# Kernel optimization log

Measured on AMD Instinct MI355X. Metric: run time of the kernel, lower is better.

Reference implementation:

```python
import jax, jax.numpy as jnp
import numpy as np

S = 95      # spatial cube size
B = 2       # batch (events)
C0 = 8      # init_conv_nplanes
C1 = 16     # planes after one downsample (inplanes*2)
K = 3       # kernel size (init conv, basic blocks, downsample)
STR = 2     # downsample stride
EPS = 1e-4  # scn BatchNorm eps
N = 40000   # total active voxels


def conv3d(x, w, stride, padding):
    # x: [B,D,H,W,Cin], w: [k,k,k,Cin,Cout]
    return jax.lax.conv_general_dilated(x, w, (stride,) * 3, padding,
                                        dimension_numbers=('NDHWC', 'DHWIO', 'NDHWC'))


def masked_bn(x, mask, gamma, beta, relu):
    # scn.BatchNorm(ReLU): per-channel stats over ACTIVE sites only
    n = jnp.maximum(mask.sum(), 1.0)
    mean = (x * mask).sum(axis=(0, 1, 2, 3)) / n
    var = (((x - mean) ** 2) * mask).sum(axis=(0, 1, 2, 3)) / n
    y = (x - mean) * jax.lax.rsqrt(var + EPS) * gamma + beta
    if relu:
        y = jnp.maximum(y, 0.0)
    return y * mask


def basic(x, mask, g1, b1, w1, g2, b2, w2):
    # pre-activation ResidualBlock_basic; submanifold convs keep the active-site mask
    y = masked_bn(x, mask, g1, b1, True)
    y = conv3d(y, w1, 1, 'SAME') * mask
    y = masked_bn(y, mask, g2, b2, True)
    y = conv3d(y, w2, 1, 'SAME') * mask
    return x + y


def downsample(x, mask, g1, b1, w1, g2, b2, w2, w3):
    # ResidualBlock_downsample: BNReLU -> {strided conv -> BNReLU -> submanifold conv} + {strided conv}
    y = masked_bn(x, mask, g1, b1, True)
    new_mask = jax.lax.reduce_window(mask, 0.0, jax.lax.max,
                                     (1, K, K, K, 1), (1, STR, STR, STR, 1), 'VALID')
    y1 = conv3d(y, w1, STR, 'VALID') * new_mask
    y1 = masked_bn(y1, new_mask, g2, b2, True)
    y1 = conv3d(y1, w2, 1, 'SAME') * new_mask
    y2 = conv3d(y, w3, STR, 'VALID') * new_mask
    return y1 + y2, new_mask


def _forward(coords, feats, w0, g0, b0,
             ba0_g1, ba0_b1, ba0_w1, ba0_g2, ba0_b2, ba0_w2,
             ba1_g1, ba1_b1, ba1_w1, ba1_g2, ba1_b2, ba1_w2,
             bo0_g1, bo0_b1, bo0_w1, bo0_g2, bo0_b2, bo0_w2,
             bo1_g1, bo1_b1, bo1_w1, bo1_g2, bo1_b2, bo1_w2,
             dn_g1, dn_b1, dn_w1, dn_g2, dn_b2, dn_w2, dn_w3,
             l1_w, l1_b, l2_w, l2_b):
    bi, xi, yi, zi = coords[:, 3], coords[:, 0], coords[:, 1], coords[:, 2]
    # scn.InputLayer: scatter (summing duplicates) into dense grid; inactive sites are exactly 0
    grid = jnp.zeros((B, S, S, S, 1), jnp.float32).at[bi, xi, yi, zi].add(feats)
    mask = jnp.zeros((B, S, S, S, 1), jnp.float32).at[bi, xi, yi, zi, 0].set(1.0)
    # ConvBNBlock: submanifold conv + BN + ReLU
    x = conv3d(grid, w0, 1, 'SAME') * mask
    x = masked_bn(x, mask, g0, b0, True)
    x = basic(x, mask, ba0_g1, ba0_b1, ba0_w1, ba0_g2, ba0_b2, ba0_w2)
    x = basic(x, mask, ba1_g1, ba1_b1, ba1_w1, ba1_g2, ba1_b2, ba1_w2)
    x, mask = downsample(x, mask, dn_g1, dn_b1, dn_w1, dn_g2, dn_b2, dn_w2, dn_w3)
    x = basic(x, mask, bo0_g1, bo0_b1, bo0_w1, bo0_g2, bo0_b2, bo0_w2)
    x = basic(x, mask, bo1_g1, bo1_b1, bo1_w1, bo1_g2, bo1_b2, bo1_w2)
    # scn.MaxPooling(full size, stride 1) + SparseToDense + squeeze: max over active sites -> [B, C1]
    pooled = jnp.where(mask > 0, x, -jnp.inf).max(axis=(1, 2, 3))
    pooled = jnp.where(jnp.isfinite(pooled), pooled, 0.0)
    h = pooled @ l1_w.T + l1_b
    return h @ l2_w.T + l2_b


def setup_inputs():
    keys = iter(jax.random.split(jax.random.key(0), 64))
    xyz = jax.random.randint(next(keys), (N, 3), 0, S, dtype=jnp.int32)
    bidx = jax.random.randint(next(keys), (N, 1), 0, B, dtype=jnp.int32)
    coords = jnp.concatenate([xyz, bidx], axis=1)
    feats = jax.random.normal(next(keys), (N, 1), dtype=jnp.float32)

    def wconv(shape):
        fan = shape[0] * shape[1] * shape[2] * shape[3]
        return jax.random.normal(next(keys), shape, jnp.float32) / np.float32(np.sqrt(fan))

    def gamma(c):
        return 1.0 + 0.1 * jax.random.normal(next(keys), (c,), jnp.float32)

    def beta(c):
        return 0.1 * jax.random.normal(next(keys), (c,), jnp.float32)

    d = {'coords': coords, 'feats': feats}
    d['w0'] = wconv((K, K, K, 1, C0)); d['g0'] = gamma(C0); d['b0'] = beta(C0)
    for name, c in [('ba0', C0), ('ba1', C0), ('bo0', C1), ('bo1', C1)]:
        d[name + '_g1'] = gamma(c); d[name + '_b1'] = beta(c); d[name + '_w1'] = wconv((K, K, K, c, c))
        d[name + '_g2'] = gamma(c); d[name + '_b2'] = beta(c); d[name + '_w2'] = wconv((K, K, K, c, c))
    d['dn_g1'] = gamma(C0); d['dn_b1'] = beta(C0); d['dn_w1'] = wconv((K, K, K, C0, C1))
    d['dn_g2'] = gamma(C1); d['dn_b2'] = beta(C1); d['dn_w2'] = wconv((K, K, K, C1, C1))
    d['dn_w3'] = wconv((K, K, K, C0, C1))
    d['l1_w'] = jax.random.normal(next(keys), (32, C1), jnp.float32) / np.float32(np.sqrt(C1))
    d['l1_b'] = beta(32)
    d['l2_w'] = jax.random.normal(next(keys), (1, 32), jnp.float32) / np.float32(np.sqrt(32))
    d['l2_b'] = beta(1)
    return d


def reference(coords, feats, w0, g0, b0,
              ba0_g1, ba0_b1, ba0_w1, ba0_g2, ba0_b2, ba0_w2,
              ba1_g1, ba1_b1, ba1_w1, ba1_g2, ba1_b2, ba1_w2,
              bo0_g1, bo0_b1, bo0_w1, bo0_g2, bo0_b2, bo0_w2,
              bo1_g1, bo1_b1, bo1_w1, bo1_g2, bo1_b2, bo1_w2,
              dn_g1, dn_b1, dn_w1, dn_g2, dn_b2, dn_w2, dn_w3,
              l1_w, l1_b, l2_w, l2_b):
    return _forward(coords, feats, w0, g0, b0,
                    ba0_g1, ba0_b1, ba0_w1, ba0_g2, ba0_b2, ba0_w2,
                    ba1_g1, ba1_b1, ba1_w1, ba1_g2, ba1_b2, ba1_w2,
                    bo0_g1, bo0_b1, bo0_w1, bo0_g2, bo0_b2, bo0_w2,
                    bo1_g1, bo1_b1, bo1_w1, bo1_g2, bo1_b2, bo1_w2,
                    dn_g1, dn_b1, dn_w1, dn_g2, dn_b2, dn_w2, dn_w3,
                    l1_w, l1_b, l2_w, l2_b)
```

## Files before the change

kernel.cpp:

```cpp
#include <hip/hip_runtime.h>
#include <cmath>

constexpr int S    = 95;
constexpr int B    = 2;
constexpr int S3   = S * S * S;
constexpr int S1   = 47;
constexpr int S13  = S1 * S1 * S1;
constexpr int NPTS = 40000;
constexpr int C0   = 8;
constexpr int C1   = 16;
constexpr float EPS = 1e-4f;
constexpr double SSCALE     = 1048576.0;
constexpr double INV_SSCALE = 1.0 / 1048576.0;
constexpr int STP = 16;

__device__ __forceinline__ unsigned encf(float f) {
    unsigned b = __float_as_uint(f);
    return (b & 0x80000000u) ? ~b : (b | 0x80000000u);
}
__device__ __forceinline__ float decf(unsigned e) {
    unsigned b = (e & 0x80000000u) ? (e ^ 0x80000000u) : ~e;
    return __uint_as_float(b);
}

template <int COUT, int SPLIT, int NW>
__device__ __forceinline__ void stats_accum(const float* acc, bool valid,
                                            float* ls, unsigned long long* stat_out) {
    constexpr int CT = COUT / SPLIT;
    float s0[CT], s1[CT];
#pragma unroll
    for (int j = 0; j < CT; ++j) { float v = valid ? acc[j] : 0.f; s0[j] = v; s1[j] = v * v; }
#pragma unroll
    for (int off = SPLIT; off < 64; off <<= 1) {
#pragma unroll
        for (int j = 0; j < CT; ++j) {
            s0[j] += __shfl_xor(s0[j], off, 64);
            s1[j] += __shfl_xor(s1[j], off, 64);
        }
    }
    int tid = threadIdx.x, lane = tid & 63, wv = tid >> 6;
    if (lane < SPLIT) {
#pragma unroll
        for (int j = 0; j < CT; ++j) {
            ls[wv * 2 * COUT + lane * CT + j]        = s0[j];
            ls[wv * 2 * COUT + COUT + lane * CT + j] = s1[j];
        }
    }
    __syncthreads();
    if (tid < 2 * COUT) {
        float t = 0.f;
#pragma unroll
        for (int w = 0; w < NW; ++w) t += ls[w * 2 * COUT + tid];
        long long q = llrint((double)t * SSCALE);
        atomicAdd(&stat_out[(size_t)tid * STP], (unsigned long long)q);
    }
}

template <int COUT, int SPLIT, int NW>
__device__ __forceinline__ void stats_accum_w(const float* acc, bool valid, int gw0,
                                              float* ls, unsigned long long* stat_out) {
    constexpr int CT = COUT / SPLIT;
    float s0[CT], s1[CT];
#pragma unroll
    for (int j = 0; j < CT; ++j) { float v = valid ? acc[j] : 0.f; s0[j] = v; s1[j] = v * v; }
#pragma unroll
    for (int off = 1; off < 64; off <<= 1) {
#pragma unroll
        for (int j = 0; j < CT; ++j) {
            s0[j] += __shfl_xor(s0[j], off, 64);
            s1[j] += __shfl_xor(s1[j], off, 64);
        }
    }
    int tid = threadIdx.x, lane = tid & 63, wv = tid >> 6;
    if (lane == 0) {
#pragma unroll
        for (int j = 0; j < CT; ++j) {
            ls[wv * 2 * CT + j]      = s0[j];
            ls[wv * 2 * CT + CT + j] = s1[j];
        }
    }
    __syncthreads();
    if (tid < 2 * COUT) {
        int part = tid / COUT;
        int ch   = tid - part * COUT;
        int qc   = ch / CT, jj = ch - qc * CT;
        float t = 0.f;
#pragma unroll
        for (int w = 0; w < NW; ++w)
            if (((gw0 + w) % SPLIT) == qc) t += ls[w * 2 * CT + part * CT + jj];
        long long q = llrint((double)t * SSCALE);
        atomicAdd(&stat_out[(size_t)tid * STP], (unsigned long long)q);
    }
}

template <int C>
__device__ __forceinline__ void bn_prologue(const unsigned long long* stat_in,
                                            const float* gamma, const float* beta,
                                            const int* cnt_bn, float* s_sc, float* s_sh) {
    int tid = threadIdx.x;
    if (tid < C) {
        double n   = fmax((double)cnt_bn[0], 1.0);
        double sm  = (double)(long long)stat_in[(size_t)tid * STP] * INV_SSCALE;
        double ssq = (double)(long long)stat_in[(size_t)(C + tid) * STP] * INV_SSCALE;
        double mean = sm / n;
        double var  = ssq / n - mean * mean;
        float sc = gamma[tid] * rsqrtf((float)var + EPS);
        s_sc[tid] = sc;
        s_sh[tid] = fmaf(-(float)mean, sc, beta[tid]);
    }
}

__global__ __launch_bounds__(256) void k_scatter(const int* __restrict__ coords,
                                                 const float* __restrict__ feats,
                                                 float* __restrict__ grid, int* __restrict__ map0,
                                                 int* __restrict__ list0, int* __restrict__ cnt0) {
    int i = blockIdx.x * 256 + threadIdx.x;
    bool valid = i < NPTS;
    int v = 0; bool own = false;
    if (valid) {
        int x = coords[i * 4 + 0], y = coords[i * 4 + 1], z = coords[i * 4 + 2], b = coords[i * 4 + 3];
        v = ((b * S + x) * S + y) * S + z;
        atomicAdd(&grid[v], feats[i]);
        own = (atomicCAS(&map0[v], 0, -1) == 0);
    }
    unsigned long long m = __ballot(own);
    int lane = threadIdx.x & 63;
    int base = 0;
    if (lane == 0) { int cw = __popcll(m); if (cw) base = atomicAdd(cnt0, cw); }
    base = __shfl(base, 0, 64);
    if (own) {
        int pos = base + __popcll(m & ((1ull << lane) - 1ull));
        list0[pos] = v;
        map0[v] = pos + 1;
    }
}

__global__ __launch_bounds__(256) void k_conv0s(const float* __restrict__ grid,
                                                const int* __restrict__ list, const int* __restrict__ cnt,
                                                const float* __restrict__ w, float* __restrict__ out,
                                                unsigned long long* __restrict__ stat_out) {
    __shared__ float wl[27 * C0];
    __shared__ float ls[4 * 2 * C0];
    const int tid = threadIdx.x;
    if (tid < 27 * C0) wl[tid] = w[tid];
    __syncthreads();
    int i = blockIdx.x * 256 + tid;
    bool valid = i < cnt[0];
    float acc[C0];
#pragma unroll
    for (int c = 0; c < C0; ++c) acc[c] = 0.f;
    if (valid) {
        int v = list[i];
        int z = v % S; int t = v / S;
        int y = t % S; t /= S;
        int x = t % S; int b = t / S;
        float gg[27];
#pragma unroll
        for (int kx = 0; kx < 3; ++kx) {
            int xx = x + kx - 1;
#pragma unroll
            for (int ky = 0; ky < 3; ++ky) {
                int yy = y + ky - 1;
#pragma unroll
                for (int kz = 0; kz < 3; ++kz) {
                    int zz = z + kz - 1;
                    bool in = (unsigned)xx < (unsigned)S && (unsigned)yy < (unsigned)S && (unsigned)zz < (unsigned)S;
                    gg[(kx * 3 + ky) * 3 + kz] = in ? grid[((b * S + xx) * S + yy) * S + zz] : 0.f;
                }
            }
        }
#pragma unroll
        for (int tap = 0; tap < 27; ++tap) {
            float g = gg[tap];
            if (g != 0.f) {
#pragma unroll
                for (int c = 0; c < C0; ++c) acc[c] = fmaf(g, wl[tap * C0 + c], acc[c]);
            }
        }
    }
    stats_accum<C0, 1, 4>(acc, valid, ls, stat_out);
    if (valid) {
#pragma unroll
        for (int c = 0; c < C0; ++c) out[(size_t)i * C0 + c] = acc[c];
    }
}

__global__ __launch_bounds__(256) void k_bn0(float* __restrict__ xs, const int* __restrict__ cnt,
                                             const unsigned long long* __restrict__ stat_in,
                                             const float* __restrict__ gamma, const float* __restrict__ beta,
                                             unsigned long long* __restrict__ stat_out) {
    __shared__ float ls[4 * 2 * C0];
    __shared__ float s_sc[C0], s_sh[C0];
    bn_prologue<C0>(stat_in, gamma, beta, cnt, s_sc, s_sh);
    __syncthreads();
    int tid = threadIdx.x;
    int i = blockIdx.x * 256 + tid;
    bool valid = i < cnt[0];
    float vals[C0];
#pragma unroll
    for (int c = 0; c < C0; ++c) vals[c] = 0.f;
    if (valid) {
#pragma unroll
        for (int c = 0; c < C0; ++c)
            vals[c] = fmaxf(fmaf(xs[(size_t)i * C0 + c], s_sc[c], s_sh[c]), 0.f);
#pragma unroll
        for (int c = 0; c < C0; ++c) xs[(size_t)i * C0 + c] = vals[c];
    }
    stats_accum<C0, 1, 4>(vals, valid, ls, stat_out);
}

template <int CIN, int COUT, int SPLIT, int SGOUT, int MODE, int TB>
__global__ __launch_bounds__(TB) void k_conv_f(const float* __restrict__ xs,
                                               const unsigned long long* __restrict__ stat_in,
                                               const float* __restrict__ gamma,
                                               const float* __restrict__ beta,
                                               const int* __restrict__ cnt_bn,
                                               const int* __restrict__ map,
                                               const int* __restrict__ list,
                                               const int* __restrict__ cnt,
                                               const float* __restrict__ w,
                                               const float* __restrict__ res,
                                               float* __restrict__ out,
                                               unsigned long long* __restrict__ stat_out,
                                               unsigned* __restrict__ pooled) {
    constexpr int CT = COUT / SPLIT;
    constexpr int NW = TB / 64;
    __shared__ float wl[27 * CIN * COUT];
    __shared__ float ls[NW * 2 * COUT];
    __shared__ float s_sc[CIN], s_sh[CIN];
    const int tid = threadIdx.x;
    const int n_act = cnt[0];
    bn_prologue<CIN>(stat_in, gamma, beta, cnt_bn, s_sc, s_sh);
    const bool blk_on = (int)(((long)blockIdx.x * TB) / SPLIT) < n_act;
    if (blk_on) {
        for (int idx = tid; idx < 27 * CIN * COUT; idx += TB) wl[idx] = w[idx];
    }
    __syncthreads();

    long gt = (long)blockIdx.x * TB + tid;
    int i = (int)(gt / SPLIT), q = (int)(gt % SPLIT);
    bool valid = i < n_act;

    float acc[CT];
#pragma unroll
    for (int j = 0; j < CT; ++j) acc[j] = 0.f;
    if (valid && res) {
#pragma unroll
        for (int j = 0; j < CT; ++j) acc[j] = res[(size_t)i * COUT + q * CT + j];
    }
    if (valid) {
        int v = list[i];
        int z = v % SGOUT; int t2 = v / SGOUT;
        int y = t2 % SGOUT; t2 /= SGOUT;
        int x = t2 % SGOUT; int b = t2 / SGOUT;
        int mm[27];
#pragma unroll
        for (int kx = 0; kx < 3; ++kx) {
            int xx = x + kx - 1;
#pragma unroll
            for (int ky = 0; ky < 3; ++ky) {
                int yy = y + ky - 1;
#pragma unroll
                for (int kz = 0; kz < 3; ++kz) {
                    int zz = z + kz - 1;
                    bool in = ((unsigned)xx < (unsigned)SGOUT && (unsigned)yy < (unsigned)SGOUT &&
                               (unsigned)zz < (unsigned)SGOUT);
                    mm[(kx * 3 + ky) * 3 + kz] = in ? map[((b * SGOUT + xx) * SGOUT + yy) * SGOUT + zz] : 0;
                }
            }
        }
#pragma unroll
        for (int tap = 0; tap < 27; ++tap) {
            int m = mm[tap];
            if (m > 0) {
                const float* row = &xs[(size_t)(m - 1) * CIN];
                float rv[CIN];
                const float4* r4 = reinterpret_cast<const float4*>(row);
#pragma unroll
                for (int u = 0; u < CIN / 4; ++u) {
                    float4 f = r4[u];
                    rv[4 * u] = f.x; rv[4 * u + 1] = f.y; rv[4 * u + 2] = f.z; rv[4 * u + 3] = f.w;
                }
                const float* wt = &wl[tap * CIN * COUT + q * CT];
#pragma unroll
                for (int ci = 0; ci < CIN; ++ci) {
                    float g = fmaxf(fmaf(rv[ci], s_sc[ci], s_sh[ci]), 0.f);
#pragma unroll
                    for (int j = 0; j < CT; ++j) acc[j] = fmaf(g, wt[ci * COUT + j], acc[j]);
                }
            }
        }
    }
    if (MODE == 1) stats_accum<COUT, SPLIT, NW>(acc, valid, ls, stat_out);
    if (valid) {
#pragma unroll
        for (int j = 0; j < CT; ++j) out[(size_t)i * COUT + q * CT + j] = acc[j];
    }
}

template <int CIN, int COUT, int SPLIT, int MODE, int TB>
__global__ __launch_bounds__(TB, 2) void k_conv_w(const float* __restrict__ xs,
                                               const unsigned long long* __restrict__ stat_in,
                                               const float* __restrict__ gamma,
                                               const float* __restrict__ beta,
                                               const int* __restrict__ cnt_bn,
                                               const int* __restrict__ map,
                                               const int* __restrict__ list,
                                               const int* __restrict__ cnt,
                                               const float* __restrict__ w,
                                               const float* __restrict__ res,
                                               float* __restrict__ out,
                                               unsigned long long* __restrict__ stat_out,
                                               unsigned* __restrict__ pooled) {
    constexpr int CT = COUT / SPLIT;
    constexpr int NW = TB / 64;
    constexpr int NV4 = CIN / 4;
    __shared__ float ls[NW * 2 * CT];
    __shared__ float s_sc[CIN], s_sh[CIN];
    __shared__ unsigned sm[B * COUT];
    const int tid  = threadIdx.x;
    const int lane = tid & 63;
    const int gw0  = blockIdx.x * NW;
    const int n_act = cnt[0];

    if (MODE == 2 && tid < B * COUT) sm[tid] = 0u;
    bn_prologue<CIN>(stat_in, gamma, beta, cnt_bn, s_sc, s_sh);
    __syncthreads();

    int gw = __builtin_amdgcn_readfirstlane(gw0 + (tid >> 6));
    int q  = gw % SPLIT;
    int c  = gw / SPLIT;
    int i  = c * 64 + lane;
    bool valid = i < n_act;

    float scr[CIN], shr[CIN];
#pragma unroll
    for (int ci = 0; ci < CIN; ++ci) { scr[ci] = s_sc[ci]; shr[ci] = s_sh[ci]; }

    float acc[CT];
#pragma unroll
    for (int j = 0; j < CT; ++j) acc[j] = 0.f;
    int b = 0;

    if (c * 64 < n_act) {
        int ii = valid ? i : (n_act - 1);
        if (valid && res) {
#pragma unroll
            for (int j = 0; j < CT; ++j) acc[j] = res[(size_t)i * COUT + q * CT + j];
        }
        int v = list[ii];
        int z = v % S1; int t2 = v / S1;
        int y = t2 % S1; t2 /= S1;
        int x = t2 % S1; b = t2 / S1;
        int mm[27];
#pragma unroll
        for (int kx = 0; kx < 3; ++kx) {
            int xx = x + kx - 1;
#pragma unroll
            for (int ky = 0; ky < 3; ++ky) {
                int yy = y + ky - 1;
#pragma unroll
                for (int kz = 0; kz < 3; ++kz) {
                    int zz = z + kz - 1;
                    bool in = (unsigned)xx < (unsigned)S1 && (unsigned)yy < (unsigned)S1 &&
                              (unsigned)zz < (unsigned)S1;
                    mm[(kx * 3 + ky) * 3 + kz] = in ? map[((b * S1 + xx) * S1 + yy) * S1 + zz] : 0;
                }
            }
        }
        auto rowp = [&](int m) {
            return reinterpret_cast<const float4*>(&xs[(size_t)(m > 0 ? m - 1 : 0) * CIN]);
        };
        float4 cr[NV4];
        {
            const float4* r = rowp(mm[0]);
#pragma unroll
            for (int u = 0; u < NV4; ++u) cr[u] = r[u];
        }
        const float* wq = w + q * CT;
        for (int tap = 0; tap < 27; ++tap) {
            float4 nr[NV4];
            {
                const float4* r = rowp(mm[tap < 26 ? tap + 1 : 26]);
#pragma unroll
                for (int u = 0; u < NV4; ++u) nr[u] = r[u];
            }
            int m = mm[tap];
            const float* wt = wq + (size_t)tap * CIN * COUT;
            float rv[CIN];
#pragma unroll
            for (int u = 0; u < NV4; ++u) {
                rv[4 * u] = cr[u].x; rv[4 * u + 1] = cr[u].y;
                rv[4 * u + 2] = cr[u].z; rv[4 * u + 3] = cr[u].w;
            }
#pragma unroll
            for (int ci = 0; ci < CIN; ++ci) {
                float g = fmaxf(fmaf(rv[ci], scr[ci], shr[ci]), 0.f);
                g = (m > 0) ? g : 0.f;
#pragma unroll
                for (int j = 0; j < CT; ++j)
                    acc[j] = fmaf(g, wt[ci * COUT + j], acc[j]);
            }
#pragma unroll
            for (int u = 0; u < NV4; ++u) cr[u] = nr[u];
        }
    }

    if (MODE == 1) {
        stats_accum_w<COUT, SPLIT, NW>(acc, valid, gw0, ls, stat_out);
        if (valid) {
#pragma unroll
            for (int j = 0; j < CT; ++j) out[(size_t)i * COUT + q * CT + j] = acc[j];
        }
    } else {
#pragma unroll
        for (int bb = 0; bb < B; ++bb) {
            float vv[CT];
#pragma unroll
            for (int j = 0; j < CT; ++j) vv[j] = (valid && b == bb) ? acc[j] : -INFINITY;
#pragma unroll
            for (int off = 1; off < 64; off <<= 1) {
#pragma unroll
                for (int j = 0; j < CT; ++j) vv[j] = fmaxf(vv[j], __shfl_xor(vv[j], off, 64));
            }
            if (lane == 0) {
#pragma unroll
                for (int j = 0; j < CT; ++j) atomicMax(&sm[bb * COUT + q * CT + j], encf(vv[j]));
            }
        }
        __syncthreads();
        if (tid < B * COUT) { unsigned e = sm[tid]; if (e) atomicMax(&pooled[tid], e); }
    }
}

template <int SPLIT, int TB>
__global__ __launch_bounds__(TB, 2) void k_conv_s2_dual(const float* __restrict__ xs,
                                                     const unsigned long long* __restrict__ stat_in,
                                                     const float* __restrict__ gamma,
                                                     const float* __restrict__ beta,
                                                     const int* __restrict__ cnt_bn,
                                                     const int* __restrict__ map0,
                                                     const int* __restrict__ list1,
                                                     const int* __restrict__ cnt1,
                                                     const float* __restrict__ w1,
                                                     const float* __restrict__ w3,
                                                     float* __restrict__ out1,
                                                     float* __restrict__ out3,
                                                     unsigned long long* __restrict__ stat_out) {
    constexpr int CIN = C0, COUT = C1, CT = COUT / SPLIT;
    constexpr int NW = TB / 64;
    constexpr int NV4 = CIN / 4;
    __shared__ float ls[NW * 2 * CT];
    __shared__ float s_sc[CIN], s_sh[CIN];
    const int tid  = threadIdx.x;
    const int lane = tid & 63;
    const int gw0  = blockIdx.x * NW;
    const int n_act = cnt1[0];
    bn_prologue<CIN>(stat_in, gamma, beta, cnt_bn, s_sc, s_sh);
    __syncthreads();

    int gw = __builtin_amdgcn_readfirstlane(gw0 + (tid >> 6));
    int q  = gw % SPLIT;
    int c  = gw / SPLIT;
    int i  = c * 64 + lane;
    bool valid = i < n_act;

    float scr[CIN], shr[CIN];
#pragma unroll
    for (int ci = 0; ci < CIN; ++ci) { scr[ci] = s_sc[ci]; shr[ci] = s_sh[ci]; }

    float acc1[CT], acc3[CT];
#pragma unroll
    for (int j = 0; j < CT; ++j) { acc1[j] = 0.f; acc3[j] = 0.f; }

    if (c * 64 < n_act) {
        int ii = valid ? i : (n_act - 1);
        int v = list1[ii];
        int z = v % S1; int t2 = v / S1;
        int y = t2 % S1; t2 /= S1;
        int x = t2 % S1; int b = t2 / S1;
        int mm[27];
#pragma unroll
        for (int kx = 0; kx < 3; ++kx)
#pragma unroll
            for (int ky = 0; ky < 3; ++ky)
#pragma unroll
                for (int kz = 0; kz < 3; ++kz)
                    mm[(kx * 3 + ky) * 3 + kz] =
                        map0[((b * S + 2 * x + kx) * S + 2 * y + ky) * S + 2 * z + kz];

        auto rowp = [&](int m) {
            return reinterpret_cast<const float4*>(&xs[(size_t)(m > 0 ? m - 1 : 0) * CIN]);
        };
        float4 cr[NV4];
        {
            const float4* r = rowp(mm[0]);
#pragma unroll
            for (int u = 0; u < NV4; ++u) cr[u] = r[u];
        }
        const float* wq1 = w1 + q * CT;
        const float* wq3 = w3 + q * CT;
        for (int tap = 0; tap < 27; ++tap) {
            float4 nr[NV4];
            {
                const float4* r = rowp(mm[tap < 26 ? tap + 1 : 26]);
#pragma unroll
                for (int u = 0; u < NV4; ++u) nr[u] = r[u];
            }
            int m = mm[tap];
            const float* wt1 = wq1 + (size_t)tap * CIN * COUT;
            const float* wt3 = wq3 + (size_t)tap * CIN * COUT;
            float rv[CIN];
#pragma unroll
            for (int u = 0; u < NV4; ++u) {
                rv[4 * u] = cr[u].x; rv[4 * u + 1] = cr[u].y;
                rv[4 * u + 2] = cr[u].z; rv[4 * u + 3] = cr[u].w;
            }
#pragma unroll
            for (int ci = 0; ci < CIN; ++ci) {
                float g = fmaxf(fmaf(rv[ci], scr[ci], shr[ci]), 0.f);
                g = (m > 0) ? g : 0.f;
#pragma unroll
                for (int j = 0; j < CT; ++j) {
                    acc1[j] = fmaf(g, wt1[ci * COUT + j], acc1[j]);
                    acc3[j] = fmaf(g, wt3[ci * COUT + j], acc3[j]);
                }
            }
#pragma unroll
            for (int u = 0; u < NV4; ++u) cr[u] = nr[u];
        }
    }
    stats_accum_w<COUT, SPLIT, NW>(acc1, valid, gw0, ls, stat_out);
    if (valid) {
#pragma unroll
        for (int j = 0; j < CT; ++j) {
            out1[(size_t)i * COUT + q * CT + j] = acc1[j];
            out3[(size_t)i * COUT + q * CT + j] = acc3[j];
        }
    }
}

__global__ __launch_bounds__(256) void k_map1(const int* __restrict__ map0, int* __restrict__ map1,
                                              int* __restrict__ list1, int* __restrict__ cnt1) {
    int v = blockIdx.x * 256 + threadIdx.x;
    bool valid = v < B * S13;
    bool act = false;
    if (valid) {
        int z = v % S1; int t = v / S1;
        int y = t % S1; t /= S1;
        int x = t % S1; int b = t / S1;
#pragma unroll
        for (int kx = 0; kx < 3; ++kx)
#pragma unroll
            for (int ky = 0; ky < 3; ++ky)
#pragma unroll
                for (int kz = 0; kz < 3; ++kz) {
                    int n = ((b * S + 2 * x + kx) * S + 2 * y + ky) * S + 2 * z + kz;
                    act = act || (map0[n] != 0);
                }
    }
    __shared__ int s_w[4];
    unsigned long long bm = __ballot(act);
    int lane = threadIdx.x & 63, wv = threadIdx.x >> 6;
    int cw = __popcll(bm);
    if (lane == 0) s_w[wv] = cw;
    __syncthreads();
    if (threadIdx.x == 0) {
        int tot = s_w[0] + s_w[1] + s_w[2] + s_w[3];
        int base = tot ? atomicAdd(cnt1, tot) : 0;
        int a = base;
        for (int k = 0; k < 4; ++k) { int c = s_w[k]; s_w[k] = a; a += c; }
    }
    __syncthreads();
    if (valid) {
        if (act) {
            int pos = s_w[wv] + __popcll(bm & ((1ull << lane) - 1ull));
            list1[pos] = v;
            map1[v] = pos + 1;
        } else {
            map1[v] = 0;
        }
    }
}

__global__ __launch_bounds__(64) void k_head(const unsigned* __restrict__ pooled,
                                             const float* __restrict__ l1w, const float* __restrict__ l1b,
                                             const float* __restrict__ l2w, const float* __restrict__ l2b,
                                             float* __restrict__ outp) {
    int t = threadIdx.x;
    int b = t >> 5, j = t & 31;
    float h = l1b[j];
#pragma unroll
    for (int c = 0; c < C1; ++c) {
        unsigned e = pooled[b * C1 + c];
        float p = (e == 0u) ? 0.f : decf(e);
        p = isfinite(p) ? p : 0.f;
        h = fmaf(l1w[j * C1 + c], p, h);
    }
    float val = l2w[j] * h;
#pragma unroll
    for (int off = 16; off > 0; off >>= 1) val += __shfl_down(val, off, 32);
    if (j == 0) outp[b] = val + l2b[0];
}

extern "C" void kernel_launch(void* const* d_in, const int* in_sizes, int n_in,
                              void* d_out, int out_size, void* d_ws, size_t ws_size,
                              hipStream_t stream) {
    const int*   coords = (const int*)  d_in[0];
    const float* feats  = (const float*)d_in[1];
    const float* w0     = (const float*)d_in[2];
    const float* g0     = (const float*)d_in[3];
    const float* b0     = (const float*)d_in[4];
    const float* ba0_g1 = (const float*)d_in[5];
    const float* ba0_b1 = (const float*)d_in[6];
    const float* ba0_w1 = (const float*)d_in[7];
    const float* ba0_g2 = (const float*)d_in[8];
    const float* ba0_b2 = (const float*)d_in[9];
    const float* ba0_w2 = (const float*)d_in[10];
    const float* ba1_g1 = (const float*)d_in[11];
    const float* ba1_b1 = (const float*)d_in[12];
    const float* ba1_w1 = (const float*)d_in[13];
    const float* ba1_g2 = (const float*)d_in[14];
    const float* ba1_b2 = (const float*)d_in[15];
    const float* ba1_w2 = (const float*)d_in[16];
    const float* bo0_g1 = (const float*)d_in[17];
    const float* bo0_b1 = (const float*)d_in[18];
    const float* bo0_w1 = (const float*)d_in[19];
    const float* bo0_g2 = (const float*)d_in[20];
    const float* bo0_b2 = (const float*)d_in[21];
    const float* bo0_w2 = (const float*)d_in[22];
    const float* bo1_g1 = (const float*)d_in[23];
    const float* bo1_b1 = (const float*)d_in[24];
    const float* bo1_w1 = (const float*)d_in[25];
    const float* bo1_g2 = (const float*)d_in[26];
    const float* bo1_b2 = (const float*)d_in[27];
    const float* bo1_w2 = (const float*)d_in[28];
    const float* dn_g1  = (const float*)d_in[29];
    const float* dn_b1  = (const float*)d_in[30];
    const float* dn_w1  = (const float*)d_in[31];
    const float* dn_g2  = (const float*)d_in[32];
    const float* dn_b2  = (const float*)d_in[33];
    const float* dn_w2  = (const float*)d_in[34];
    const float* dn_w3  = (const float*)d_in[35];
    const float* l1_w   = (const float*)d_in[36];
    const float* l1_b   = (const float*)d_in[37];
    const float* l2_w   = (const float*)d_in[38];
    const float* l2_b   = (const float*)d_in[39];

    char* p = (char*)d_ws;
    auto take = [&](size_t elems) -> float* {
        float* r = (float*)p;
        p += ((elems * 4 + 255) / 256) * 256;
        return r;
    };
    float* grid    = take((size_t)B * S3);
    int*   map0    = (int*)take((size_t)B * S3);
    float* x0      = take((size_t)NPTS * C0);
    float* t0      = take((size_t)NPTS * C0);
    int*   map1    = (int*)take((size_t)B * S13);
    float* t1      = take((size_t)B * S13 * C1);
    float* r1      = take((size_t)B * S13 * C1);
    float* x1      = take((size_t)B * S13 * C1);
    unsigned long long* stats = (unsigned long long*)take(11 * 32 * STP * 2);
    unsigned* pooled = (unsigned*)take(B * C1);
    int*   cnt     = (int*)take(16);
    char* zero_end = p;
    int*   list0   = (int*)take(NPTS);
    int*   list1   = (int*)take((size_t)B * S13);
    int* cnt0 = cnt;
    int* cnt1 = cnt + 1;
    auto G = [&](int g) { return stats + (size_t)g * 32 * STP; };

    hipMemsetAsync(grid, 0, (size_t)((char*)x0 - (char*)grid), stream);
    hipMemsetAsync(stats, 0, (size_t)(zero_end - (char*)stats), stream);

    constexpr int TBW = 512;
    constexpr int SPL = 2;
    const int NB_C0 = (NPTS + 255) / 256;
    const int NB_L0 = (NPTS * 4 + 255) / 256;
    const int NB_M1 = (B * S13 + 255) / 256;
    const int CHUNKS = (B * S13 + 63) / 64;
    const int NB_W  = (CHUNKS * SPL + (TBW / 64) - 1) / (TBW / 64);

    k_scatter<<<NB_C0, 256, 0, stream>>>(coords, feats, grid, map0, list0, cnt0);
    k_conv0s<<<NB_C0, 256, 0, stream>>>(grid, list0, cnt0, w0, x0, G(0));
    k_bn0<<<NB_C0, 256, 0, stream>>>(x0, cnt0, G(0), g0, b0, G(1));

    k_conv_f<C0, C0, 4, S, 1, 256><<<NB_L0, 256, 0, stream>>>(x0, G(1), ba0_g1, ba0_b1, cnt0,
                                                              map0, list0, cnt0, ba0_w1, nullptr, t0, G(2), nullptr);
    k_conv_f<C0, C0, 4, S, 1, 256><<<NB_L0, 256, 0, stream>>>(t0, G(2), ba0_g2, ba0_b2, cnt0,
                                                              map0, list0, cnt0, ba0_w2, x0, x0, G(3), nullptr);

    k_conv_f<C0, C0, 4, S, 1, 256><<<NB_L0, 256, 0, stream>>>(x0, G(3), ba1_g1, ba1_b1, cnt0,
                                                              map0, list0, cnt0, ba1_w1, nullptr, t0, G(4), nullptr);
    k_conv_f<C0, C0, 4, S, 1, 256><<<NB_L0, 256, 0, stream>>>(t0, G(4), ba1_g2, ba1_b2, cnt0,
                                                              map0, list0, cnt0, ba1_w2, x0, x0, G(5), nullptr);

    k_map1<<<NB_M1, 256, 0, stream>>>(map0, map1, list1, cnt1);
    k_conv_s2_dual<SPL, TBW><<<NB_W, TBW, 0, stream>>>(x0, G(5), dn_g1, dn_b1, cnt0,
                                                       map0, list1, cnt1, dn_w1, dn_w3, t1, r1, G(6));
    k_conv_w<C1, C1, SPL, 1, TBW><<<NB_W, TBW, 0, stream>>>(t1, G(6), dn_g2, dn_b2, cnt1,
                                                            map1, list1, cnt1, dn_w2, r1, x1, G(7), nullptr);

    k_conv_w<C1, C1, SPL, 1, TBW><<<NB_W, TBW, 0, stream>>>(x1, G(7), bo0_g1, bo0_b1, cnt1,
                                                            map1, list1, cnt1, bo0_w1, nullptr, t1, G(8), nullptr);
    k_conv_w<C1, C1, SPL, 1, TBW><<<NB_W, TBW, 0, stream>>>(t1, G(8), bo0_g2, bo0_b2, cnt1,
                                                            map1, list1, cnt1, bo0_w2, x1, x1, G(9), nullptr);

    k_conv_w<C1, C1, SPL, 1, TBW><<<NB_W, TBW, 0, stream>>>(x1, G(9), bo1_g1, bo1_b1, cnt1,
                                                            map1, list1, cnt1, bo1_w1, nullptr, t1, G(10), nullptr);
    k_conv_w<C1, C1, SPL, 2, TBW><<<NB_W, TBW, 0, stream>>>(t1, G(10), bo1_g2, bo1_b2, cnt1,
                                                            map1, list1, cnt1, bo1_w2, x1, nullptr, nullptr, pooled);

    k_head<<<1, 64, 0, stream>>>(pooled, l1_w, l1_b, l2_w, l2_b, (float*)d_out);
}
```

Before: 364.4 us.

## Split BN+ReLU into standalone kernels with zero-row padding and XCD block remap

Moves the BN+ReLU applied to each gathered neighbour row out of the conv kernels into separate elementwise kernels. Each activation buffer gains a zero row at index 0, so missing neighbours (map value 0) read zeros and the conv loops drop the mask and BN math. The conv_w and s2_dual loops are also fully unrolled with a two-deep prefetch buffer, and conv_w remaps block IDs across the 8 XCDs. The trade-off is roughly ten extra kernel launches and an additional read/write pass over the activations, in exchange for removing 27x redundant BN work per output.

```diff
diff --git a/kernel.cpp b/kernel.cpp
--- a/kernel.cpp
+++ b/kernel.cpp
@@ -110,6 +110,13 @@
     }
 }
 
+__global__ __launch_bounds__(64) void k_zero(float* x0, float* t0, float* ya,
+                                             float* t1, float* r1, float* x1, float* y1) {
+    int t = threadIdx.x;
+    if (t < C0) { x0[t] = 0.f; t0[t] = 0.f; ya[t] = 0.f; }
+    if (t < C1) { t1[t] = 0.f; r1[t] = 0.f; x1[t] = 0.f; y1[t] = 0.f; }
+}
+
 __global__ __launch_bounds__(256) void k_scatter(const int* __restrict__ coords,
                                                  const float* __restrict__ feats,
                                                  float* __restrict__ grid, int* __restrict__ map0,
@@ -181,7 +188,7 @@
     stats_accum<C0, 1, 4>(acc, valid, ls, stat_out);
     if (valid) {
 #pragma unroll
-        for (int c = 0; c < C0; ++c) out[(size_t)i * C0 + c] = acc[c];
+        for (int c = 0; c < C0; ++c) out[(size_t)(i + 1) * C0 + c] = acc[c];
     }
 }
 
@@ -202,35 +209,46 @@
     if (valid) {
 #pragma unroll
         for (int c = 0; c < C0; ++c)
-            vals[c] = fmaxf(fmaf(xs[(size_t)i * C0 + c], s_sc[c], s_sh[c]), 0.f);
-#pragma unroll
-        for (int c = 0; c < C0; ++c) xs[(size_t)i * C0 + c] = vals[c];
+            vals[c] = fmaxf(fmaf(xs[(size_t)(i + 1) * C0 + c], s_sc[c], s_sh[c]), 0.f);
+#pragma unroll
+        for (int c = 0; c < C0; ++c) xs[(size_t)(i + 1) * C0 + c] = vals[c];
     }
     stats_accum<C0, 1, 4>(vals, valid, ls, stat_out);
 }
 
-template <int CIN, int COUT, int SPLIT, int SGOUT, int MODE, int TB>
+template <int C>
+__global__ __launch_bounds__(256) void k_bn_act(const float* __restrict__ xin,
+                                                float* __restrict__ yout,
+                                                const int* __restrict__ cnt,
+                                                const unsigned long long* __restrict__ stat_in,
+                                                const float* __restrict__ gamma,
+                                                const float* __restrict__ beta) {
+    __shared__ float s_sc[C], s_sh[C];
+    bn_prologue<C>(stat_in, gamma, beta, cnt, s_sc, s_sh);
+    __syncthreads();
+    int i = blockIdx.x * 256 + threadIdx.x;
+    if (i >= cnt[0]) return;
+    size_t r = (size_t)(i + 1) * C;
+#pragma unroll
+    for (int c = 0; c < C; ++c)
+        yout[r + c] = fmaxf(fmaf(xin[r + c], s_sc[c], s_sh[c]), 0.f);
+}
+
+template <int CIN, int COUT, int SPLIT, int SGOUT, int TB>
 __global__ __launch_bounds__(TB) void k_conv_f(const float* __restrict__ xs,
-                                               const unsigned long long* __restrict__ stat_in,
-                                               const float* __restrict__ gamma,
-                                               const float* __restrict__ beta,
-                                               const int* __restrict__ cnt_bn,
                                                const int* __restrict__ map,
                                                const int* __restrict__ list,
                                                const int* __restrict__ cnt,
                                                const float* __restrict__ w,
                                                const float* __restrict__ res,
                                                float* __restrict__ out,
-                                               unsigned long long* __restrict__ stat_out,
-                                               unsigned* __restrict__ pooled) {
+                                               unsigned long long* __restrict__ stat_out) {
     constexpr int CT = COUT / SPLIT;
     constexpr int NW = TB / 64;
     __shared__ float wl[27 * CIN * COUT];
     __shared__ float ls[NW * 2 * COUT];
-    __shared__ float s_sc[CIN], s_sh[CIN];
     const int tid = threadIdx.x;
     const int n_act = cnt[0];
-    bn_prologue<CIN>(stat_in, gamma, beta, cnt_bn, s_sc, s_sh);
     const bool blk_on = (int)(((long)blockIdx.x * TB) / SPLIT) < n_act;
     if (blk_on) {
         for (int idx = tid; idx < 27 * CIN * COUT; idx += TB) wl[idx] = w[idx];
@@ -246,7 +264,7 @@
     for (int j = 0; j < CT; ++j) acc[j] = 0.f;
     if (valid && res) {
 #pragma unroll
-        for (int j = 0; j < CT; ++j) acc[j] = res[(size_t)i * COUT + q * CT + j];
+        for (int j = 0; j < CT; ++j) acc[j] = res[(size_t)(i + 1) * COUT + q * CT + j];
     }
     if (valid) {
         int v = list[i];
@@ -273,7 +291,7 @@
         for (int tap = 0; tap < 27; ++tap) {
             int m = mm[tap];
             if (m > 0) {
-                const float* row = &xs[(size_t)(m - 1) * CIN];
+                const float* row = &xs[(size_t)m * CIN];
                 float rv[CIN];
                 const float4* r4 = reinterpret_cast<const float4*>(row);
 #pragma unroll
@@ -284,26 +302,22 @@
                 const float* wt = &wl[tap * CIN * COUT + q * CT];
 #pragma unroll
                 for (int ci = 0; ci < CIN; ++ci) {
-                    float g = fmaxf(fmaf(rv[ci], s_sc[ci], s_sh[ci]), 0.f);
+                    float g = rv[ci];
 #pragma unroll
                     for (int j = 0; j < CT; ++j) acc[j] = fmaf(g, wt[ci * COUT + j], acc[j]);
                 }
             }
         }
     }
-    if (MODE == 1) stats_accum<COUT, SPLIT, NW>(acc, valid, ls, stat_out);
-    if (valid) {
-#pragma unroll
-        for (int j = 0; j < CT; ++j) out[(size_t)i * COUT + q * CT + j] = acc[j];
+    stats_accum<COUT, SPLIT, NW>(acc, valid, ls, stat_out);
+    if (valid) {
+#pragma unroll
+        for (int j = 0; j < CT; ++j) out[(size_t)(i + 1) * COUT + q * CT + j] = acc[j];
     }
 }
 
 template <int CIN, int COUT, int SPLIT, int MODE, int TB>
 __global__ __launch_bounds__(TB, 2) void k_conv_w(const float* __restrict__ xs,
-                                               const unsigned long long* __restrict__ stat_in,
-                                               const float* __restrict__ gamma,
-                                               const float* __restrict__ beta,
-                                               const int* __restrict__ cnt_bn,
                                                const int* __restrict__ map,
                                                const int* __restrict__ list,
                                                const int* __restrict__ cnt,
@@ -316,16 +330,19 @@
     constexpr int NW = TB / 64;
     constexpr int NV4 = CIN / 4;
     __shared__ float ls[NW * 2 * CT];
-    __shared__ float s_sc[CIN], s_sh[CIN];
     __shared__ unsigned sm[B * COUT];
     const int tid  = threadIdx.x;
     const int lane = tid & 63;
-    const int gw0  = blockIdx.x * NW;
     const int n_act = cnt[0];
 
     if (MODE == 2 && tid < B * COUT) sm[tid] = 0u;
-    bn_prologue<CIN>(stat_in, gamma, beta, cnt_bn, s_sc, s_sh);
-    __syncthreads();
+    __syncthreads();
+
+    int nwg = gridDim.x;
+    int qq = nwg >> 3, rr = nwg & 7;
+    int xcd = blockIdx.x & 7, idx = blockIdx.x >> 3;
+    int bid = (xcd < rr ? xcd * (qq + 1) : rr * (qq + 1) + (xcd - rr) * qq) + idx;
+    const int gw0 = bid * NW;
 
     int gw = __builtin_amdgcn_readfirstlane(gw0 + (tid >> 6));
     int q  = gw % SPLIT;
@@ -333,10 +350,6 @@
     int i  = c * 64 + lane;
     bool valid = i < n_act;
 
-    float scr[CIN], shr[CIN];
-#pragma unroll
-    for (int ci = 0; ci < CIN; ++ci) { scr[ci] = s_sc[ci]; shr[ci] = s_sh[ci]; }
-
     float acc[CT];
 #pragma unroll
     for (int j = 0; j < CT; ++j) acc[j] = 0.f;
@@ -346,7 +359,7 @@
         int ii = valid ? i : (n_act - 1);
         if (valid && res) {
 #pragma unroll
-            for (int j = 0; j < CT; ++j) acc[j] = res[(size_t)i * COUT + q * CT + j];
+            for (int j = 0; j < CT; ++j) acc[j] = res[(size_t)(i + 1) * COUT + q * CT + j];
         }
         int v = list[ii];
         int z = v % S1; int t2 = v / S1;
@@ -368,41 +381,35 @@
                 }
             }
         }
-        auto rowp = [&](int m) {
-            return reinterpret_cast<const float4*>(&xs[(size_t)(m > 0 ? m - 1 : 0) * CIN]);
-        };
-        float4 cr[NV4];
+        float4 pb[2][NV4];
         {
-            const float4* r = rowp(mm[0]);
-#pragma unroll
-            for (int u = 0; u < NV4; ++u) cr[u] = r[u];
+            const float4* r0 = reinterpret_cast<const float4*>(&xs[(size_t)mm[0] * CIN]);
+            const float4* r1p = reinterpret_cast<const float4*>(&xs[(size_t)mm[1] * CIN]);
+#pragma unroll
+            for (int u = 0; u < NV4; ++u) { pb[0][u] = r0[u]; pb[1][u] = r1p[u]; }
         }
         const float* wq = w + q * CT;
+#pragma unroll
         for (int tap = 0; tap < 27; ++tap) {
-            float4 nr[NV4];
-            {
-                const float4* r = rowp(mm[tap < 26 ? tap + 1 : 26]);
-#pragma unroll
-                for (int u = 0; u < NV4; ++u) nr[u] = r[u];
-            }
-            int m = mm[tap];
+            float rv[CIN];
+#pragma unroll
+            for (int u = 0; u < NV4; ++u) {
+                float4 f = pb[tap & 1][u];
+                rv[4 * u] = f.x; rv[4 * u + 1] = f.y; rv[4 * u + 2] = f.z; rv[4 * u + 3] = f.w;
+            }
+            if (tap + 2 < 27) {
+                const float4* r = reinterpret_cast<const float4*>(&xs[(size_t)mm[tap + 2] * CIN]);
+#pragma unroll
+                for (int u = 0; u < NV4; ++u) pb[tap & 1][u] = r[u];
+            }
             const float* wt = wq + (size_t)tap * CIN * COUT;
-            float rv[CIN];
-#pragma unroll
-            for (int u = 0; u < NV4; ++u) {
-                rv[4 * u] = cr[u].x; rv[4 * u + 1] = cr[u].y;
-                rv[4 * u + 2] = cr[u].z; rv[4 * u + 3] = cr[u].w;
-            }
 #pragma unroll
             for (int ci = 0; ci < CIN; ++ci) {
-                float g = fmaxf(fmaf(rv[ci], scr[ci], shr[ci]), 0.f);
-                g = (m > 0) ? g : 0.f;
+                float g = rv[ci];
 #pragma unroll
                 for (int j = 0; j < CT; ++j)
                     acc[j] = fmaf(g, wt[ci * COUT + j], acc[j]);
             }
-#pragma unroll
-            for (int u = 0; u < NV4; ++u) cr[u] = nr[u];
         }
     }
 
@@ -410,7 +417,7 @@
         stats_accum_w<COUT, SPLIT, NW>(acc, valid, gw0, ls, stat_out);
         if (valid) {
 #pragma unroll
-            for (int j = 0; j < CT; ++j) out[(size_t)i * COUT + q * CT + j] = acc[j];
+            for (int j = 0; j < CT; ++j) out[(size_t)(i + 1) * COUT + q * CT + j] = acc[j];
         }
     } else {
 #pragma unroll
@@ -435,10 +442,6 @@
 
 template <int SPLIT, int TB>
 __global__ __launch_bounds__(TB, 2) void k_conv_s2_dual(const float* __restrict__ xs,
-                                                     const unsigned long long* __restrict__ stat_in,
-                                                     const float* __restrict__ gamma,
-                                                     const float* __restrict__ beta,
-                                                     const int* __restrict__ cnt_bn,
                                                      const int* __restrict__ map0,
                                                      const int* __restrict__ list1,
                                                      const int* __restrict__ cnt1,
@@ -451,23 +454,16 @@
     constexpr int NW = TB / 64;
     constexpr int NV4 = CIN / 4;
     __shared__ float ls[NW * 2 * CT];
-    __shared__ float s_sc[CIN], s_sh[CIN];
     const int tid  = threadIdx.x;
     const int lane = tid & 63;
     const int gw0  = blockIdx.x * NW;
     const int n_act = cnt1[0];
-    bn_prologue<CIN>(stat_in, gamma, beta, cnt_bn, s_sc, s_sh);
-    __syncthreads();
 
     int gw = __builtin_amdgcn_readfirstlane(gw0 + (tid >> 6));
     int q  = gw % SPLIT;
     int c  = gw / SPLIT;
     int i  = c * 64 + lane;
     bool valid = i < n_act;
-
-    float scr[CIN], shr[CIN];
-#pragma unroll
-    for (int ci = 0; ci < CIN; ++ci) { scr[ci] = s_sc[ci]; shr[ci] = s_sh[ci]; }
 
     float acc1[CT], acc3[CT];
 #pragma unroll
@@ -489,53 +485,47 @@
                     mm[(kx * 3 + ky) * 3 + kz] =
                         map0[((b * S + 2 * x + kx) * S + 2 * y + ky) * S + 2 * z + kz];
 
-        auto rowp = [&](int m) {
-            return reinterpret_cast<const float4*>(&xs[(size_t)(m > 0 ? m - 1 : 0) * CIN]);
-        };
-        float4 cr[NV4];
+        float4 pb[2][NV4];
         {
-            const float4* r = rowp(mm[0]);
-#pragma unroll
-            for (int u = 0; u < NV4; ++u) cr[u] = r[u];
+            const float4* r0 = reinterpret_cast<const float4*>(&xs[(size_t)mm[0] * CIN]);
+            const float4* r1p = reinterpret_cast<const float4*>(&xs[(size_t)mm[1] * CIN]);
+#pragma unroll
+            for (int u = 0; u < NV4; ++u) { pb[0][u] = r0[u]; pb[1][u] = r1p[u]; }
         }
         const float* wq1 = w1 + q * CT;
         const float* wq3 = w3 + q * CT;
+#pragma unroll
         for (int tap = 0; tap < 27; ++tap) {
-            float4 nr[NV4];
-            {
-                const float4* r = rowp(mm[tap < 26 ? tap + 1 : 26]);
-#pragma unroll
-                for (int u = 0; u < NV4; ++u) nr[u] = r[u];
-            }
-            int m = mm[tap];
+            float rv[CIN];
+#pragma unroll
+            for (int u = 0; u < NV4; ++u) {
+                float4 f = pb[tap & 1][u];
+                rv[4 * u] = f.x; rv[4 * u + 1] = f.y; rv[4 * u + 2] = f.z; rv[4 * u + 3] = f.w;
+            }
+            if (tap + 2 < 27) {
+                const float4* r = reinterpret_cast<const float4*>(&xs[(size_t)mm[tap + 2] * CIN]);
+#pragma unroll
+                for (int u = 0; u < NV4; ++u) pb[tap & 1][u] = r[u];
+            }
             const float* wt1 = wq1 + (size_t)tap * CIN * COUT;
             const float* wt3 = wq3 + (size_t)tap * CIN * COUT;
-            float rv[CIN];
-#pragma unroll
-            for (int u = 0; u < NV4; ++u) {
-                rv[4 * u] = cr[u].x; rv[4 * u + 1] = cr[u].y;
-                rv[4 * u + 2] = cr[u].z; rv[4 * u + 3] = cr[u].w;
-            }
 #pragma unroll
             for (int ci = 0; ci < CIN; ++ci) {
-                float g = fmaxf(fmaf(rv[ci], scr[ci], shr[ci]), 0.f);
-                g = (m > 0) ? g : 0.f;
+                float g = rv[ci];
 #pragma unroll
                 for (int j = 0; j < CT; ++j) {
                     acc1[j] = fmaf(g, wt1[ci * COUT + j], acc1[j]);
                     acc3[j] = fmaf(g, wt3[ci * COUT + j], acc3[j]);
                 }
             }
-#pragma unroll
-            for (int u = 0; u < NV4; ++u) cr[u] = nr[u];
         }
     }
     stats_accum_w<COUT, SPLIT, NW>(acc1, valid, gw0, ls, stat_out);
     if (valid) {
 #pragma unroll
         for (int j = 0; j < CT; ++j) {
-            out1[(size_t)i * COUT + q * CT + j] = acc1[j];
-            out3[(size_t)i * COUT + q * CT + j] = acc3[j];
+            out1[(size_t)(i + 1) * COUT + q * CT + j] = acc1[j];
+            out3[(size_t)(i + 1) * COUT + q * CT + j] = acc3[j];
         }
     }
 }
@@ -655,12 +645,14 @@
     };
     float* grid    = take((size_t)B * S3);
     int*   map0    = (int*)take((size_t)B * S3);
-    float* x0      = take((size_t)NPTS * C0);
-    float* t0      = take((size_t)NPTS * C0);
+    float* x0      = take((size_t)(NPTS + 1) * C0);
+    float* t0      = take((size_t)(NPTS + 1) * C0);
+    float* ya      = take((size_t)(NPTS + 1) * C0);
     int*   map1    = (int*)take((size_t)B * S13);
-    float* t1      = take((size_t)B * S13 * C1);
-    float* r1      = take((size_t)B * S13 * C1);
-    float* x1      = take((size_t)B * S13 * C1);
+    float* t1      = take((size_t)(B * S13 + 1) * C1);
+    float* r1      = take((size_t)(B * S13 + 1) * C1);
+    float* x1      = take((size_t)(B * S13 + 1) * C1);
+    float* y1      = take((size_t)(B * S13 + 1) * C1);
     unsigned long long* stats = (unsigned long long*)take(11 * 32 * STP * 2);
     unsigned* pooled = (unsigned*)take(B * C1);
     int*   cnt     = (int*)take(16);
@@ -682,35 +674,36 @@
     const int CHUNKS = (B * S13 + 63) / 64;
     const int NB_W  = (CHUNKS * SPL + (TBW / 64) - 1) / (TBW / 64);
 
+    k_zero<<<1, 64, 0, stream>>>(x0, t0, ya, t1, r1, x1, y1);
     k_scatter<<<NB_C0, 256, 0, stream>>>(coords, feats, grid, map0, list0, cnt0);
     k_conv0s<<<NB_C0, 256, 0, stream>>>(grid, list0, cnt0, w0, x0, G(0));
     k_bn0<<<NB_C0, 256, 0, stream>>>(x0, cnt0, G(0), g0, b0, G(1));
 
-    k_conv_f<C0, C0, 4, S, 1, 256><<<NB_L0, 256, 0, stream>>>(x0, G(1), ba0_g1, ba0_b1, cnt0,
-                                                              map0, list0, cnt0, ba0_w1, nullptr, t0, G(2), nullptr);
-    k_conv_f<C0, C0, 4, S, 1, 256><<<NB_L0, 256, 0, stream>>>(t0, G(2), ba0_g2, ba0_b2, cnt0,
-                                                              map0, list0, cnt0, ba0_w2, x0, x0, G(3), nullptr);
-
-    k_conv_f<C0, C0, 4, S, 1, 256><<<NB_L0, 256, 0, stream>>>(x0, G(3), ba1_g1, ba1_b1, cnt0,
-                                                              map0, list0, cnt0, ba1_w1, nullptr, t0, G(4), nullptr);
-    k_conv_f<C0, C0, 4, S, 1, 256><<<NB_L0, 256, 0, stream>>>(t0, G(4), ba1_g2, ba1_b2, cnt0,
-                                                              map0, list0, cnt0, ba1_w2, x0, x0, G(5), nullptr);
+    k_bn_act<C0><<<NB_C0, 256, 0, stream>>>(x0, ya, cnt0, G(1), ba0_g1, ba0_b1);
+    k_conv_f<C0, C0, 4, S, 256><<<NB_L0, 256, 0, stream>>>(ya, map0, list0, cnt0, ba0_w1, nullptr, t0, G(2));
+    k_bn_act<C0><<<NB_C0, 256, 0, stream>>>(t0, t0, cnt0, G(2), ba0_g2, ba0_b2);
+    k_conv_f<C0, C0, 4, S, 256><<<NB_L0, 256, 0, stream>>>(t0, map0, list0, cnt0, ba0_w2, x0, x0, G(3));
+
+    k_bn_act<C0><<<NB_C0, 256, 0, stream>>>(x0, ya, cnt0, G(3), ba1_g1, ba1_b1);
+    k_conv_f<C0, C0, 4, S, 256><<<NB_L0, 256, 0, stream>>>(ya, map0, list0, cnt0, ba1_w1, nullptr, t0, G(4));
+    k_bn_act<C0><<<NB_C0, 256, 0, stream>>>(t0, t0, cnt0, G(4), ba1_g2, ba1_b2);
+    k_conv_f<C0, C0, 4, S, 256><<<NB_L0, 256, 0, stream>>>(t0, map0, list0, cnt0, ba1_w2, x0, x0, G(5));
 
     k_map1<<<NB_M1, 256, 0, stream>>>(map0, map1, list1, cnt1);
-    k_conv_s2_dual<SPL, TBW><<<NB_W, TBW, 0, stream>>>(x0, G(5), dn_g1, dn_b1, cnt0,
-                                                       map0, list1, cnt1, dn_w1, dn_w3, t1, r1, G(6));
-    k_conv_w<C1, C1, SPL, 1, TBW><<<NB_W, TBW, 0, stream>>>(t1, G(6), dn_g2, dn_b2, cnt1,
-                                                            map1, list1, cnt1, dn_w2, r1, x1, G(7), nullptr);
-
-    k_conv_w<C1, C1, SPL, 1, TBW><<<NB_W, TBW, 0, stream>>>(x1, G(7), bo0_g1, bo0_b1, cnt1,
-                                                            map1, list1, cnt1, bo0_w1, nullptr, t1, G(8), nullptr);
-    k_conv_w<C1, C1, SPL, 1, TBW><<<NB_W, TBW, 0, stream>>>(t1, G(8), bo0_g2, bo0_b2, cnt1,
-                                                            map1, list1, cnt1, bo0_w2, x1, x1, G(9), nullptr);
-
-    k_conv_w<C1, C1, SPL, 1, TBW><<<NB_W, TBW, 0, stream>>>(x1, G(9), bo1_g1, bo1_b1, cnt1,
-                                                            map1, list1, cnt1, bo1_w1, nullptr, t1, G(10), nullptr);
-    k_conv_w<C1, C1, SPL, 2, TBW><<<NB_W, TBW, 0, stream>>>(t1, G(10), bo1_g2, bo1_b2, cnt1,
-                                                            map1, list1, cnt1, bo1_w2, x1, nullptr, nullptr, pooled);
+    k_bn_act<C0><<<NB_C0, 256, 0, stream>>>(x0, ya, cnt0, G(5), dn_g1, dn_b1);
+    k_conv_s2_dual<SPL, TBW><<<NB_W, TBW, 0, stream>>>(ya, map0, list1, cnt1, dn_w1, dn_w3, t1, r1, G(6));
+    k_bn_act<C1><<<NB_M1, 256, 0, stream>>>(t1, t1, cnt1, G(6), dn_g2, dn_b2);
+    k_conv_w<C1, C1, SPL, 1, TBW><<<NB_W, TBW, 0, stream>>>(t1, map1, list1, cnt1, dn_w2, r1, x1, G(7), nullptr);
+
+    k_bn_act<C1><<<NB_M1, 256, 0, stream>>>(x1, y1, cnt1, G(7), bo0_g1, bo0_b1);
+    k_conv_w<C1, C1, SPL, 1, TBW><<<NB_W, TBW, 0, stream>>>(y1, map1, list1, cnt1, bo0_w1, nullptr, t1, G(8), nullptr);
+    k_bn_act<C1><<<NB_M1, 256, 0, stream>>>(t1, t1, cnt1, G(8), bo0_g2, bo0_b2);
+    k_conv_w<C1, C1, SPL, 1, TBW><<<NB_W, TBW, 0, stream>>>(t1, map1, list1, cnt1, bo0_w2, x1, x1, G(9), nullptr);
+
+    k_bn_act<C1><<<NB_M1, 256, 0, stream>>>(x1, y1, cnt1, G(9), bo1_g1, bo1_b1);
+    k_conv_w<C1, C1, SPL, 1, TBW><<<NB_W, TBW, 0, stream>>>(y1, map1, list1, cnt1, bo1_w1, nullptr, t1, G(10), nullptr);
+    k_bn_act<C1><<<NB_M1, 256, 0, stream>>>(t1, t1, cnt1, G(10), bo1_g2, bo1_b2);
+    k_conv_w<C1, C1, SPL, 2, TBW><<<NB_W, TBW, 0, stream>>>(t1, map1, list1, cnt1, bo1_w2, x1, nullptr, nullptr, pooled);
 
     k_head<<<1, 64, 0, stream>>>(pooled, l1_w, l1_b, l2_w, l2_b, (float*)d_out);
 }
```

New measurement: 596.1 us. 1.64x slower.
